# Kernel optimization log

Measured on AMD Instinct MI355X. Metric: run time of the kernel, lower is better.

The kernel has to match this reference:

```python
import jax, jax.numpy as jnp
import numpy as np

K = 20            # neighbors
C = 21            # num_classes
P = 16            # patch_size
NROWS = 14        # img_size // patch_size
H = NROWS * P     # 224
TEMP = 1.0        # temperature


def setup_inputs() -> dict:
    key = jax.random.key(0)
    k1, k2, k3 = jax.random.split(key, 3)
    test_feature = jax.random.normal(k1, (8, 196, 384), dtype=jnp.float32)
    train_features = jax.random.normal(k2, (384, 50000), dtype=jnp.float32)
    train_labels = jax.random.randint(k3, (256, 50000), 0, C, dtype=jnp.int32)
    return {"test_feature": test_feature, "train_features": train_features,
            "train_labels": train_labels}


def reference(test_feature, train_features, train_labels):
    bs = test_feature.shape[0]
    # similarity: [bs, num_patches, N_train]
    sim = jnp.einsum('bpd,dn->bpn', test_feature, train_features)
    sim_k, idx = jax.lax.top_k(sim, K)              # [bs, 196, K]
    # gather neighbor patch labels: train_labels [P^2, N] -> [bs, 196, K, P^2]
    nb = train_labels.T[idx]
    # make_grid with nrow=NROWS, padding=0: assemble patches into [bs, K, H, H]
    nb = nb.reshape(bs, NROWS, NROWS, K, P, P)
    nb = nb.transpose(0, 3, 1, 4, 2, 5).reshape(bs, K, H, H)
    nb = nb.transpose(0, 2, 3, 1)                   # [bs, H, H, K]
    # weighted majority vote: nearest-upsample similarities 14x14 -> 224x224
    w = sim_k.reshape(bs, NROWS, NROWS, K)
    w = jnp.repeat(jnp.repeat(w, P, axis=1), P, axis=2)   # [bs, H, H, K]
    w = jax.nn.softmax(w / TEMP, axis=-1)
    # one-hot vote expressed as scatter-add over classes (same math, no
    # [bs,H,H,K,C] materialization)
    rows = jnp.arange(bs * H * H)
    vote = jnp.zeros((bs * H * H, C), dtype=w.dtype)
    vote = vote.at[rows[:, None], nb.reshape(bs * H * H, K)].add(
        w.reshape(bs * H * H, K))
    vote = vote.reshape(bs, H, H, C)
    pred = jnp.argmax(vote, axis=-1)                # [bs, H, H] int
    return pred
```

## Files before the change

kernel.cpp:

```cpp
#include <hip/hip_runtime.h>
#include <float.h>

#define N_TRAIN 50000
#define NPAD    50176
#define NBLK    392
#define NBLK2   196
#define MPAD    1792
#define DDIM    384
#define M_ROWS  1568
#define KNN     20
#define K2      24
#define SELMAX  64
#define NCLS    21
#define CAPBUF  768
#define CBMAX   256

typedef __attribute__((ext_vector_type(8))) short bf16x8;
typedef __attribute__((ext_vector_type(4))) float f32x4;

#define GLOAD_LDS16(gp, lp) \
  __builtin_amdgcn_global_load_lds((const __attribute__((address_space(1))) void*)(gp), \
                                   (__attribute__((address_space(3))) void*)(lp), 16, 0, 0)
#define WAITVM(N) asm volatile("s_waitcnt vmcnt(" #N ")" ::: "memory")

static __device__ __forceinline__ unsigned short f2bf(float f) {
  unsigned int u = __float_as_uint(f);
  unsigned int r = (u + 0x7fffu + ((u >> 16) & 1u)) >> 16;
  return (unsigned short)r;
}
static __device__ __forceinline__ unsigned int flip32(unsigned int u) {
  return (u & 0x80000000u) ? ~u : (u | 0x80000000u);
}

__global__ __launch_bounds__(256) void transpose_labels(const int* __restrict__ labels,
                                                        unsigned char* __restrict__ labT) {
  __shared__ int tile[64][65];
  const int t  = threadIdx.x;
  const int c0 = blockIdx.x * 64;
  const int r0 = blockIdx.y * 64;
#pragma unroll
  for (int i = 0; i < 16; ++i) {
    int idx = i * 256 + t;
    int r = idx >> 6, c = idx & 63;
    int cc = c0 + c;
    tile[r][c] = (cc < N_TRAIN) ? labels[(size_t)(r0 + r) * N_TRAIN + cc] : 0;
  }
  __syncthreads();
#pragma unroll
  for (int i = 0; i < 16; ++i) {
    int idx = i * 256 + t;
    int c = idx >> 6, r = idx & 63;
    int cc = c0 + c;
    if (cc < N_TRAIN) labT[(size_t)cc * 256 + r0 + r] = (unsigned char)tile[r][c];
  }
}

__global__ __launch_bounds__(256) void conv_bf16A(const float* __restrict__ test,
                                                  unsigned short* __restrict__ bf16A) {
  int idx = blockIdx.x * 256 + threadIdx.x;
  if (idx >= MPAD * DDIM) return;
  int row = idx / DDIM;
  bf16A[idx] = (row < M_ROWS) ? f2bf(test[idx]) : (unsigned short)0;
}

__global__ __launch_bounds__(256) void trans_train_fused(const float* __restrict__ train,
                                                         unsigned short* __restrict__ bhT,
                                                         float* __restrict__ trainT) {
  __shared__ float tile[64][65];
  const int t  = threadIdx.x;
  const int c0 = blockIdx.x * 64;
  const int r0 = blockIdx.y * 64;
#pragma unroll
  for (int i = 0; i < 16; ++i) {
    int idx = i * 256 + t;
    int r = idx >> 6, c = idx & 63;
    int cc = c0 + c;
    tile[r][c] = (cc < N_TRAIN) ? train[(size_t)(r0 + r) * N_TRAIN + cc] : 0.f;
  }
  __syncthreads();
#pragma unroll
  for (int i = 0; i < 16; ++i) {
    int idx = i * 256 + t;
    int c = idx >> 6, r = idx & 63;
    int cc = c0 + c;
    float v = tile[r][c];
    bhT[(size_t)cc * DDIM + r0 + r] = f2bf(v);
    if (cc < N_TRAIN) trainT[(size_t)cc * DDIM + r0 + r] = v;
  }
}

__global__ __launch_bounds__(512, 2) void mfma_gemm(const unsigned short* __restrict__ bf16A,
                                                    const unsigned short* __restrict__ bhT,
                                                    unsigned short* __restrict__ keybuf,
                                                    unsigned short* __restrict__ blkmax) {
  extern __shared__ unsigned short lds16[];
  const int t = threadIdx.x;

  const int flat = blockIdx.x;
  const int xcd = flat & 7, jj = flat >> 3;
  const int wg = (xcd < 4 ? xcd * 172 : 688 + (xcd - 4) * 171) + jj;
  const int mblk = wg % 7, nblk = wg / 7;
  const int m0 = mblk * 256, n0 = nblk * 256;

  const int wid = t >> 6, lane = t & 63;
  const int wr = wid >> 2, wc = wid & 3;
  const int l15 = lane & 15, l4 = lane >> 4;
  const int srow = t >> 3;
  const int sx   = (t & 7) ^ (srow & 7);

  f32x4 acc[8][4];
  const f32x4 zero = {0.f, 0.f, 0.f, 0.f};
#pragma unroll
  for (int f = 0; f < 8; ++f)
#pragma unroll
    for (int n = 0; n < 4; ++n) acc[f][n] = zero;

#define STAGE_HALF(tk, h)                                                          \
  {                                                                                \
    const int slot_ = (tk) & 1;                                                    \
    _Pragma("unroll")                                                              \
    for (int j2 = 2 * (h); j2 < 2 * (h) + 2; ++j2) {                               \
      GLOAD_LDS16(bf16A + (size_t)(m0 + j2 * 64 + srow) * DDIM + (tk) * 64 + sx * 8, \
                  &lds16[slot_ * 16384 + j2 * 4096 + wid * 512]);                  \
      GLOAD_LDS16(bhT + (size_t)(n0 + j2 * 64 + srow) * DDIM + (tk) * 64 + sx * 8, \
                  &lds16[32768 + slot_ * 16384 + j2 * 4096 + wid * 512]);          \
    }                                                                              \
  }

  STAGE_HALF(0, 0);
  STAGE_HALF(0, 1);

#pragma unroll
  for (int p = 0; p < 12; ++p) {
    const int tk = p >> 1, h = p & 1;
    if (tk + 1 < 6) STAGE_HALF(tk + 1, h);
    if (p >= 10)      { WAITVM(0); }
    else if (h == 0)  { WAITVM(4); }
    else              { WAITVM(8); }
    __builtin_amdgcn_s_barrier();
    asm volatile("" ::: "memory");

    const int aBase = (tk & 1) * 16384;
    const int bBase = 32768 + (tk & 1) * 16384;
    const int physc = ((h * 4 + l4) ^ (l15 & 7)) * 8;
    bf16x8 a[8], b[4];
#pragma unroll
    for (int f = 0; f < 8; ++f)
      a[f] = *(const bf16x8*)&lds16[aBase + (wr * 128 + f * 16 + l15) * 64 + physc];
#pragma unroll
    for (int n = 0; n < 4; ++n)
      b[n] = *(const bf16x8*)&lds16[bBase + (wc * 64 + n * 16 + l15) * 64 + physc];

    __builtin_amdgcn_s_setprio(1);
#pragma unroll
    for (int f = 0; f < 8; ++f)
#pragma unroll
      for (int n = 0; n < 4; ++n)
        acc[f][n] = __builtin_amdgcn_mfma_f32_16x16x32_bf16(a[f], b[n], acc[f][n], 0, 0, 0);
    __builtin_amdgcn_s_setprio(0);

    asm volatile("s_waitcnt lgkmcnt(0)" ::: "memory");
    __builtin_amdgcn_s_barrier();
  }

  __syncthreads();
#pragma unroll
  for (int f = 0; f < 8; ++f) {
    const int row0 = wr * 128 + f * 16 + l4 * 4;
#pragma unroll
    for (int n = 0; n < 4; ++n) {
      const int col = wc * 64 + n * 16 + l15;
      const int cl = col >> 3, ce = col & 7;
#pragma unroll
      for (int r = 0; r < 4; ++r) {
        const int rr = row0 + r;
        unsigned int k16 = flip32(__float_as_uint(acc[f][n][r])) >> 16;
        lds16[rr * 256 + ((cl ^ (rr & 31)) << 3) + ce] = (unsigned short)k16;
      }
    }
  }
  __syncthreads();

  const bool boundary = (n0 + 256 > N_TRAIN);
#pragma unroll
  for (int i = 0; i < 16; ++i) {
    int idx = i * 512 + t;
    int row = idx >> 5;
    int cL  = idx & 31;
    uint4 v = *(uint4*)&lds16[row * 256 + ((cL ^ (row & 31)) << 3)];
    int c8 = cL * 8;
    if (boundary) {
      int nv = N_TRAIN - (n0 + c8);
      v.x &= ((0 < nv) ? 0x0000FFFFu : 0u) | ((1 < nv) ? 0xFFFF0000u : 0u);
      v.y &= ((2 < nv) ? 0x0000FFFFu : 0u) | ((3 < nv) ? 0xFFFF0000u : 0u);
      v.z &= ((4 < nv) ? 0x0000FFFFu : 0u) | ((5 < nv) ? 0xFFFF0000u : 0u);
      v.w &= ((6 < nv) ? 0x0000FFFFu : 0u) | ((7 < nv) ? 0xFFFF0000u : 0u);
    }
    unsigned int mx = v.x & 0xFFFFu;
    mx = max(mx, v.x >> 16); mx = max(mx, v.y & 0xFFFFu); mx = max(mx, v.y >> 16);
    mx = max(mx, v.z & 0xFFFFu); mx = max(mx, v.z >> 16);
    mx = max(mx, v.w & 0xFFFFu); mx = max(mx, v.w >> 16);
    mx = max(mx, (unsigned int)__shfl_xor((int)mx, 1));
    mx = max(mx, (unsigned int)__shfl_xor((int)mx, 2));
    mx = max(mx, (unsigned int)__shfl_xor((int)mx, 4));
    mx = max(mx, (unsigned int)__shfl_xor((int)mx, 8));
    const int grow = m0 + row;
    if (grow < M_ROWS) {
      if ((lane & 15) == 0) {
        int half = (lane >> 4) & 1;
        blkmax[(size_t)grow * NBLK + nblk * 2 + half] = (unsigned short)mx;
      }
      *(uint4*)&keybuf[(size_t)grow * NPAD + n0 + c8] = v;
    }
  }
#undef STAGE_HALF
}

__global__ __launch_bounds__(256) void tail_fused(const unsigned short* __restrict__ keybuf,
                                                  const unsigned short* __restrict__ blkmax,
                                                  const float* __restrict__ test,
                                                  const float* __restrict__ trainT,
                                                  const unsigned char* __restrict__ labT,
                                                  int* __restrict__ out) {
  const int t = threadIdx.x, m = blockIdx.x;
  __shared__ unsigned short bm[NBLK];
  __shared__ int clist[CBMAX];
  __shared__ int ccnt;
  __shared__ unsigned int smax[256];
  __shared__ unsigned int sbuf[CAPBUF];
  __shared__ short srk[CAPBUF];
  __shared__ unsigned int scnt, sTauA, sTau;
  __shared__ int sC2;
  __shared__ int selC[SELMAX];
  __shared__ double rvs[SELMAX];
  __shared__ double sv2[SELMAX];
  __shared__ int    si2[SELMAX];
  __shared__ double earr[KNN];
  __shared__ double wv[KNN];
  __shared__ int    wi[KNN];

  if (t == 0) { ccnt = 0; scnt = 0u; sC2 = 0; }
  for (int i = t; i < NBLK; i += 256) bm[i] = blkmax[(size_t)m * NBLK + i];
  __syncthreads();

  for (int i = t; i < NBLK; i += 256) {
    unsigned short v = bm[i];
    int cgt = 0;
    for (int j = 0; j < NBLK; ++j) cgt += (bm[j] > v) ? 1 : 0;
    if (cgt < K2) { int p = atomicAdd(&ccnt, 1); if (p < CBMAX) clist[p] = i; }
  }
  __syncthreads();
  const int CB = min(ccnt, CBMAX);
  const int TOT = CB * 128;

  unsigned int tmx = 0u;
  for (int i = t; i < TOT; i += 256) {
    int col = clist[i >> 7] * 128 + (i & 127);
    unsigned int k = keybuf[(size_t)m * NPAD + col];
    if (k > tmx) tmx = k;
  }
  smax[t] = (tmx << 8) | (unsigned int)(255 - t);
  __syncthreads();
  {
    unsigned int myc = smax[t];
    int rnk = 0;
    for (int j = 0; j < 256; ++j) rnk += (smax[j] > myc) ? 1 : 0;
    if (rnk == K2 - 1) sTauA = myc >> 8;
  }
  __syncthreads();
  const unsigned int tauB = sTauA;

  for (int i = t; i < TOT; i += 256) {
    int col = clist[i >> 7] * 128 + (i & 127);
    unsigned int k = keybuf[(size_t)m * NPAD + col];
    if (k >= tauB) {
      unsigned int p = atomicAdd(&scnt, 1u);
      if (p < CAPBUF) sbuf[p] = (k << 16) | (unsigned int)(0xFFFF - col);
    }
  }
  __syncthreads();
  const int C = (int)min(scnt, (unsigned int)CAPBUF);

  for (int s = t; s < C; s += 256) {
    unsigned int e = sbuf[s];
    int rk = 0;
    for (int j = 0; j < C; ++j) rk += (sbuf[j] > e) ? 1 : 0;
    srk[s] = (short)rk;
    if (rk == K2 - 1) sTau = e >> 16;
  }
  __syncthreads();
  const unsigned int tau = sTau;
  for (int s = t; s < C; s += 256) {
    unsigned int e = sbuf[s];
    int rk = (int)srk[s];
    if ((e >> 16) >= tau && rk < SELMAX) {
      selC[rk] = 0xFFFF - (int)(e & 0xFFFFu);
      atomicMax(&sC2, rk + 1);
    }
  }
  __syncthreads();
  const int C2 = sC2 < SELMAX ? sC2 : SELMAX;

  const int wid = t >> 6, lane = t & 63;
  float tr[DDIM / 64];
#pragma unroll
  for (int dd = 0; dd < DDIM / 64; ++dd)
    tr[dd] = test[(size_t)m * DDIM + dd * 64 + lane];
#pragma unroll 1
  for (int c = wid; c < C2; c += 4) {
    const float* Tc = trainT + (size_t)selC[c] * DDIM;
    double s = 0.0;
#pragma unroll
    for (int dd = 0; dd < DDIM / 64; ++dd)
      s += (double)tr[dd] * (double)Tc[dd * 64 + lane];
#pragma unroll
    for (int off = 32; off > 0; off >>= 1) s += __shfl_xor(s, off);
    if (lane == 0) rvs[c] = s;
  }
  __syncthreads();

  if (t < C2) {
    double v = rvs[t]; int id = selC[t];
    int r = 0;
    for (int n = 0; n < C2; ++n)
      r += (rvs[n] > v || (rvs[n] == v && selC[n] < id)) ? 1 : 0;
    sv2[r] = v; si2[r] = id;
  }
  __syncthreads();

  if (t < KNN) earr[t] = exp(sv2[t] - sv2[0]);
  __syncthreads();
  if (t < KNN) {
    double ssum = 0.0;
    for (int k = 0; k < KNN; ++k) ssum += earr[k];
    wv[t] = earr[t] / ssum;
    wi[t] = si2[t];
  }
  __syncthreads();

  unsigned int packed[5];
#pragma unroll
  for (int q = 0; q < 5; ++q) {
    unsigned int p = 0;
#pragma unroll
    for (int j = 0; j < 4; ++j)
      p |= (unsigned int)labT[(size_t)wi[q * 4 + j] * 256 + t] << (8 * j);
    packed[q] = p;
  }
  double best = -1.0; int bc = 0;
#pragma unroll 1
  for (int c = 0; c < NCLS; ++c) {
    double s = 0.0;
#pragma unroll
    for (int k = 0; k < KNN; ++k) {
      unsigned int lab = (packed[k >> 2] >> ((k & 3) * 8)) & 255u;
      s += (lab == (unsigned int)c) ? wv[k] : 0.0;
    }
    if (s > best) { best = s; bc = c; }
  }
  const int b = m / 196, p = m % 196;
  const int py = p / 14, px = p % 14;
  const int i = t >> 4, j = t & 15;
  out[((size_t)b * 224 + py * 16 + i) * 224 + px * 16 + j] = bc;
}

extern "C" void kernel_launch(void* const* d_in, const int* in_sizes, int n_in,
                              void* d_out, int out_size, void* d_ws, size_t ws_size,
                              hipStream_t stream) {
  const float* test  = (const float*)d_in[0];
  const float* train = (const float*)d_in[1];
  const int* labels  = (const int*)d_in[2];
  int* out = (int*)d_out;
  char* ws = (char*)d_ws;

  unsigned char*  labT    = (unsigned char*)ws;
  unsigned short* bf16A   = (unsigned short*)(ws + 12800000);
  unsigned short* bhT     = (unsigned short*)(ws + 14176256);
  unsigned short* keybuf  = (unsigned short*)(ws + 52711424);
  float*          trainT  = (float*)(ws + 210063360);
  unsigned short* blkmax  = (unsigned short*)(ws + 286863360);

  transpose_labels<<<dim3(782, 4), 256, 0, stream>>>(labels, labT);
  conv_bf16A<<<dim3((MPAD * DDIM + 255) / 256), 256, 0, stream>>>(test, bf16A);
  trans_train_fused<<<dim3(784, 6), 256, 0, stream>>>(train, bhT, trainT);
  mfma_gemm<<<dim3(7 * NBLK2), 512, 131072, stream>>>(bf16A, bhT, keybuf, blkmax);
  tail_fused<<<dim3(M_ROWS), 256, 0, stream>>>(keybuf, blkmax, test, trainT, labT, out);
}
```

Baseline: 261.0 us.

## Pre-pack GEMM operands in MFMA fragment layout and load directly from global

The bf16 A and B operands are now written in a pre-swizzled layout that matches the MFMA 16x16x32 register fragments. This lets the GEMM kernel load fragments straight from global memory with no LDS staging, double buffering or barriers. The GEMM tile shrinks from 256x256 with 512 threads to 128x256 with 256 threads, and only a static LDS buffer is kept for the epilogue. The aim is to remove LDS traffic and synchronisation, at the cost of losing explicit load/compute overlap and relying on L2/cache reuse for operand loads.

```diff
diff --git a/kernel.cpp b/kernel.cpp
--- a/kernel.cpp
+++ b/kernel.cpp
@@ -4,7 +4,6 @@
 #define N_TRAIN 50000
 #define NPAD    50176
 #define NBLK    392
-#define NBLK2   196
 #define MPAD    1792
 #define DDIM    384
 #define M_ROWS  1568
@@ -18,11 +17,6 @@
 typedef __attribute__((ext_vector_type(8))) short bf16x8;
 typedef __attribute__((ext_vector_type(4))) float f32x4;
 
-#define GLOAD_LDS16(gp, lp) \
-  __builtin_amdgcn_global_load_lds((const __attribute__((address_space(1))) void*)(gp), \
-                                   (__attribute__((address_space(3))) void*)(lp), 16, 0, 0)
-#define WAITVM(N) asm volatile("s_waitcnt vmcnt(" #N ")" ::: "memory")
-
 static __device__ __forceinline__ unsigned short f2bf(float f) {
   unsigned int u = __float_as_uint(f);
   unsigned int r = (u + 0x7fffu + ((u >> 16) & 1u)) >> 16;
@@ -55,16 +49,21 @@
   }
 }
 
-__global__ __launch_bounds__(256) void conv_bf16A(const float* __restrict__ test,
-                                                  unsigned short* __restrict__ bf16A) {
-  int idx = blockIdx.x * 256 + threadIdx.x;
-  if (idx >= MPAD * DDIM) return;
-  int row = idx / DDIM;
-  bf16A[idx] = (row < M_ROWS) ? f2bf(test[idx]) : (unsigned short)0;
+__global__ __launch_bounds__(256) void conv_Apack(const float* __restrict__ test,
+                                                  unsigned short* __restrict__ Apack) {
+  int o = blockIdx.x * 256 + threadIdx.x;
+  if (o >= (MPAD / 16) * 12 * 512) return;
+  int j = o & 7;
+  int l = (o >> 3) & 63;
+  int kcmt = o >> 9;
+  int kc = kcmt % 12, mt = kcmt / 12;
+  int row = mt * 16 + (l & 15);
+  int k = kc * 32 + (l >> 4) * 8 + j;
+  Apack[o] = (row < M_ROWS) ? f2bf(test[(size_t)row * DDIM + k]) : (unsigned short)0;
 }
 
 __global__ __launch_bounds__(256) void trans_train_fused(const float* __restrict__ train,
-                                                         unsigned short* __restrict__ bhT,
+                                                         unsigned short* __restrict__ Bpack,
                                                          float* __restrict__ trainT) {
   __shared__ float tile[64][65];
   const int t  = threadIdx.x;
@@ -79,34 +78,48 @@
   }
   __syncthreads();
 #pragma unroll
+  for (int it = 0; it < 2; ++it) {
+    int u = it * 256 + t;
+    int c = u & 63, koctL = u >> 6;
+    int col = c0 + c;
+    int koct = (r0 >> 3) + koctL;
+    int kc = koct >> 2, l4 = koct & 3;
+    int nt = col >> 4, l15 = col & 15;
+    size_t base = ((size_t)(nt * 12 + kc) * 64 + l4 * 16 + l15) * 8;
+    ushort4 h0, h1;
+    h0.x = f2bf(tile[koctL * 8 + 0][c]); h0.y = f2bf(tile[koctL * 8 + 1][c]);
+    h0.z = f2bf(tile[koctL * 8 + 2][c]); h0.w = f2bf(tile[koctL * 8 + 3][c]);
+    h1.x = f2bf(tile[koctL * 8 + 4][c]); h1.y = f2bf(tile[koctL * 8 + 5][c]);
+    h1.z = f2bf(tile[koctL * 8 + 6][c]); h1.w = f2bf(tile[koctL * 8 + 7][c]);
+    *(ushort4*)&Bpack[base]     = h0;
+    *(ushort4*)&Bpack[base + 4] = h1;
+  }
+#pragma unroll
   for (int i = 0; i < 16; ++i) {
     int idx = i * 256 + t;
     int c = idx >> 6, r = idx & 63;
     int cc = c0 + c;
-    float v = tile[r][c];
-    bhT[(size_t)cc * DDIM + r0 + r] = f2bf(v);
-    if (cc < N_TRAIN) trainT[(size_t)cc * DDIM + r0 + r] = v;
-  }
-}
-
-__global__ __launch_bounds__(512, 2) void mfma_gemm(const unsigned short* __restrict__ bf16A,
-                                                    const unsigned short* __restrict__ bhT,
+    if (cc < N_TRAIN) trainT[(size_t)cc * DDIM + r0 + r] = tile[r][c];
+  }
+}
+
+__global__ __launch_bounds__(256, 2) void mfma_gemm(const unsigned short* __restrict__ Apack,
+                                                    const unsigned short* __restrict__ Bpack,
                                                     unsigned short* __restrict__ keybuf,
                                                     unsigned short* __restrict__ blkmax) {
-  extern __shared__ unsigned short lds16[];
+  __shared__ unsigned short ct[128 * 256];
   const int t = threadIdx.x;
 
   const int flat = blockIdx.x;
-  const int xcd = flat & 7, jj = flat >> 3;
-  const int wg = (xcd < 4 ? xcd * 172 : 688 + (xcd - 4) * 171) + jj;
-  const int mblk = wg % 7, nblk = wg / 7;
-  const int m0 = mblk * 256, n0 = nblk * 256;
-
-  const int wid = t >> 6, lane = t & 63;
-  const int wr = wid >> 2, wc = wid & 3;
+  const int wg = (flat & 7) * 343 + (flat >> 3);
+  const int mblk = wg % 14, nblk = wg / 14;
+  const int m0 = mblk * 128, n0 = nblk * 256;
+
+  const int wc = t >> 6, lane = t & 63;
   const int l15 = lane & 15, l4 = lane >> 4;
-  const int srow = t >> 3;
-  const int sx   = (t & 7) ^ (srow & 7);
+
+  const unsigned short* Ab = Apack + (size_t)(mblk * 8) * 12 * 512;
+  const unsigned short* Bb = Bpack + (size_t)(nblk * 16 + wc * 4) * 12 * 512;
 
   f32x4 acc[8][4];
   const f32x4 zero = {0.f, 0.f, 0.f, 0.f};
@@ -115,58 +128,24 @@
 #pragma unroll
     for (int n = 0; n < 4; ++n) acc[f][n] = zero;
 
-#define STAGE_HALF(tk, h)                                                          \
-  {                                                                                \
-    const int slot_ = (tk) & 1;                                                    \
-    _Pragma("unroll")                                                              \
-    for (int j2 = 2 * (h); j2 < 2 * (h) + 2; ++j2) {                               \
-      GLOAD_LDS16(bf16A + (size_t)(m0 + j2 * 64 + srow) * DDIM + (tk) * 64 + sx * 8, \
-                  &lds16[slot_ * 16384 + j2 * 4096 + wid * 512]);                  \
-      GLOAD_LDS16(bhT + (size_t)(n0 + j2 * 64 + srow) * DDIM + (tk) * 64 + sx * 8, \
-                  &lds16[32768 + slot_ * 16384 + j2 * 4096 + wid * 512]);          \
-    }                                                                              \
-  }
-
-  STAGE_HALF(0, 0);
-  STAGE_HALF(0, 1);
-
-#pragma unroll
-  for (int p = 0; p < 12; ++p) {
-    const int tk = p >> 1, h = p & 1;
-    if (tk + 1 < 6) STAGE_HALF(tk + 1, h);
-    if (p >= 10)      { WAITVM(0); }
-    else if (h == 0)  { WAITVM(4); }
-    else              { WAITVM(8); }
-    __builtin_amdgcn_s_barrier();
-    asm volatile("" ::: "memory");
-
-    const int aBase = (tk & 1) * 16384;
-    const int bBase = 32768 + (tk & 1) * 16384;
-    const int physc = ((h * 4 + l4) ^ (l15 & 7)) * 8;
+  for (int kc = 0; kc < 12; ++kc) {
     bf16x8 a[8], b[4];
 #pragma unroll
     for (int f = 0; f < 8; ++f)
-      a[f] = *(const bf16x8*)&lds16[aBase + (wr * 128 + f * 16 + l15) * 64 + physc];
+      a[f] = *(const bf16x8*)&Ab[((size_t)(f * 12 + kc) * 64 + lane) * 8];
 #pragma unroll
     for (int n = 0; n < 4; ++n)
-      b[n] = *(const bf16x8*)&lds16[bBase + (wc * 64 + n * 16 + l15) * 64 + physc];
-
-    __builtin_amdgcn_s_setprio(1);
+      b[n] = *(const bf16x8*)&Bb[((size_t)(n * 12 + kc) * 64 + lane) * 8];
 #pragma unroll
     for (int f = 0; f < 8; ++f)
 #pragma unroll
       for (int n = 0; n < 4; ++n)
         acc[f][n] = __builtin_amdgcn_mfma_f32_16x16x32_bf16(a[f], b[n], acc[f][n], 0, 0, 0);
-    __builtin_amdgcn_s_setprio(0);
-
-    asm volatile("s_waitcnt lgkmcnt(0)" ::: "memory");
-    __builtin_amdgcn_s_barrier();
-  }
-
-  __syncthreads();
+  }
+
 #pragma unroll
   for (int f = 0; f < 8; ++f) {
-    const int row0 = wr * 128 + f * 16 + l4 * 4;
+    const int row0 = f * 16 + l4 * 4;
 #pragma unroll
     for (int n = 0; n < 4; ++n) {
       const int col = wc * 64 + n * 16 + l15;
@@ -175,7 +154,7 @@
       for (int r = 0; r < 4; ++r) {
         const int rr = row0 + r;
         unsigned int k16 = flip32(__float_as_uint(acc[f][n][r])) >> 16;
-        lds16[rr * 256 + ((cl ^ (rr & 31)) << 3) + ce] = (unsigned short)k16;
+        ct[rr * 256 + ((cl ^ (rr & 31)) << 3) + ce] = (unsigned short)k16;
       }
     }
   }
@@ -184,10 +163,10 @@
   const bool boundary = (n0 + 256 > N_TRAIN);
 #pragma unroll
   for (int i = 0; i < 16; ++i) {
-    int idx = i * 512 + t;
+    int idx = i * 256 + t;
     int row = idx >> 5;
     int cL  = idx & 31;
-    uint4 v = *(uint4*)&lds16[row * 256 + ((cL ^ (row & 31)) << 3)];
+    uint4 v = *(uint4*)&ct[row * 256 + ((cL ^ (row & 31)) << 3)];
     int c8 = cL * 8;
     if (boundary) {
       int nv = N_TRAIN - (n0 + c8);
@@ -213,7 +192,6 @@
       *(uint4*)&keybuf[(size_t)grow * NPAD + n0 + c8] = v;
     }
   }
-#undef STAGE_HALF
 }
 
 __global__ __launch_bounds__(256) void tail_fused(const unsigned short* __restrict__ keybuf,
@@ -374,15 +352,15 @@
   char* ws = (char*)d_ws;
 
   unsigned char*  labT    = (unsigned char*)ws;
-  unsigned short* bf16A   = (unsigned short*)(ws + 12800000);
-  unsigned short* bhT     = (unsigned short*)(ws + 14176256);
+  unsigned short* Apack   = (unsigned short*)(ws + 12800000);
+  unsigned short* Bpack   = (unsigned short*)(ws + 14176256);
   unsigned short* keybuf  = (unsigned short*)(ws + 52711424);
   float*          trainT  = (float*)(ws + 210063360);
   unsigned short* blkmax  = (unsigned short*)(ws + 286863360);
 
   transpose_labels<<<dim3(782, 4), 256, 0, stream>>>(labels, labT);
-  conv_bf16A<<<dim3((MPAD * DDIM + 255) / 256), 256, 0, stream>>>(test, bf16A);
-  trans_train_fused<<<dim3(784, 6), 256, 0, stream>>>(train, bhT, trainT);
-  mfma_gemm<<<dim3(7 * NBLK2), 512, 131072, stream>>>(bf16A, bhT, keybuf, blkmax);
+  conv_Apack<<<dim3(2688), 256, 0, stream>>>(test, Apack);
+  trans_train_fused<<<dim3(784, 6), 256, 0, stream>>>(train, Bpack, trainT);
+  mfma_gemm<<<dim3(2744), 256, 0, stream>>>(Apack, Bpack, keybuf, blkmax);
   tail_fused<<<dim3(M_ROWS), 256, 0, stream>>>(keybuf, blkmax, test, trainT, labT, out);
 }
```

Result: no change. 257.9 us (-1.2%).
